# Kernel optimization log

Measured on AMD Instinct MI355X. Metric: run time of the kernel, lower is better.

Reference implementation:

```python
import jax, jax.numpy as jnp
import numpy as np

NUM_HEADS = 4
MIN_NORM = 1e-8


def setup_inputs() -> dict:
    key = jax.random.key(0)
    k1, k2 = jax.random.split(key)
    N, D = 4096, 129  # D = out_channels + 1 (Lorentz time coord + space)
    query_input = jax.random.normal(k1, (N, D), dtype=jnp.float32)
    source_input = jax.random.normal(k2, (N, D), dtype=jnp.float32)
    scale = jnp.full((1,), np.sqrt(128.0), dtype=jnp.float32)  # sqrt(out_channels)
    bias = jnp.zeros((), dtype=jnp.float32)
    return {"query_input": query_input, "source_input": source_input,
            "scale": scale, "bias": bias}


def _lorentz_self_inner(x):
    # <x,x>_L = -x0^2 + ||x_rest||^2, keepdim on last axis
    return -x[..., :1] ** 2 + jnp.sum(x[..., 1:] ** 2, axis=-1, keepdims=True)


def _mid_point_normalize(ave):
    # mid_point denominator: sqrt(clamp_min(|-<ave,ave>_L|, 1e-8))
    denom = jnp.sqrt(jnp.clip(jnp.abs(-_lorentz_self_inner(ave)), MIN_NORM, None))
    return ave / denom


def reference(query_input, source_input, scale, bias):
    H = NUM_HEADS
    N, D = query_input.shape
    # stack identical copies per head (module stacks the raw inputs H times)
    q = jnp.broadcast_to(query_input[None], (H, N, D))   # [H,N,D]
    k = jnp.broadcast_to(source_input[None], (H, N, D))  # [H,N,D]
    v = k
    # cinner: negate time component of q, then matmul with k^T
    qm = jnp.concatenate([-q[..., :1], q[..., 1:]], axis=-1)
    att = 2.0 + 2.0 * jnp.einsum('hnd,hmd->hnm', qm, k)  # [H,N,N]
    att = att / scale + bias
    att = jax.nn.softmax(att, axis=-1)
    # mid_point with weights: ave = att @ v, then Lorentz normalization
    ave = jnp.einsum('hnm,hmd->hnd', att, v)              # [H,N,D]
    out = _mid_point_normalize(ave)
    # transpose to [N,H,D], mid_point without weights = mean over heads
    out = jnp.transpose(out, (1, 0, 2))                   # [N,H,D]
    ave2 = jnp.mean(out, axis=-2)                         # [N,D]
    return _mid_point_normalize(ave2)
```

## Files before the change

kernel.cpp:

```cpp
#include <hip/hip_runtime.h>
#include <math.h>


typedef __attribute__((ext_vector_type(8))) _Float16 f16x8;
typedef __attribute__((ext_vector_type(8))) short short8;
typedef __attribute__((ext_vector_type(4))) float f32x4;

#define NQ 4096
#define DD 129
#define BM 16
#define NWAVE 8
#define NT 512
#define TILE 32
#define NSPLIT 2
#define KVSEG (NQ / NSPLIT)
#define NSTEP (KVSEG / (NWAVE * TILE))
#define NQG (NQ / BM)

#define WS_KH   ((size_t)0)
#define WS_VT   ((size_t)1 << 20)
#define WS_K128 ((size_t)2 << 20)
#define WS_OP   ((size_t)3 << 20)
#define WS_MLA  ((size_t)7 << 20)

__device__ __forceinline__ short f2h_bits(float x) {
  _Float16 h = (_Float16)x;
  return *reinterpret_cast<short*>(&h);
}

__global__ __launch_bounds__(256) void prepass(
    const float* __restrict__ Kg,
    short* __restrict__ Kh, short* __restrict__ VT, float* __restrict__ K128)
{
  __shared__ short tile[32][128];
  const int t  = threadIdx.x;
  const int j0 = blockIdx.x * 32;

#pragma unroll
  for (int i = 0; i < 2; ++i) {
    const int idx = t + 256 * i;
    const int r   = idx >> 4;
    const int d0  = (idx & 15) * 8;
    const float* src = Kg + (size_t)(j0 + r) * DD + d0;
    short8 sv;
#pragma unroll
    for (int e = 0; e < 8; ++e) {
      const short s = f2h_bits(src[e]);
      sv[e] = s;
      tile[r][d0 + e] = s;
    }
    *reinterpret_cast<short8*>(Kh + (size_t)(j0 + r) * 128 + d0) = sv;
  }
  if (t < 32) K128[j0 + t] = Kg[(size_t)(j0 + t) * DD + 128];
  __syncthreads();

  {
    const int d = t >> 1, half = t & 1;
    short v[16];
#pragma unroll
    for (int i = 0; i < 16; ++i) {
      const int p = 16 * half + i;
      const int g = p >> 3, e = p & 7;
      const int j = (e < 4) ? (4 * g + e) : (16 + 4 * g + (e - 4));
      v[i] = tile[j][d];
    }
    short8 s0, s1;
#pragma unroll
    for (int i = 0; i < 8; ++i) { s0[i] = v[i]; s1[i] = v[8 + i]; }
    short* dst = VT + (size_t)d * NQ + j0 + 16 * half;
    *reinterpret_cast<short8*>(dst)     = s0;
    *reinterpret_cast<short8*>(dst + 8) = s1;
  }
}

__global__ __launch_bounds__(NT, 4) void attn_split(
    const float* __restrict__ Qg,
    const short* __restrict__ Kh, const short* __restrict__ VT,
    const float* __restrict__ K128,
    const float* __restrict__ scale_p, const float* __restrict__ bias_p,
    float* __restrict__ OP, float* __restrict__ MLA)
{
  __shared__ float OwS[4][BM * 128];
  __shared__ float mS[NWAVE][BM], lS[NWAVE][BM], aS[NWAVE][BM];

  const int bid = blockIdx.x;
  const int xcd = bid & 7;
  const int sp  = xcd & 1;
  const int qg  = ((xcd >> 1) << 6) + (bid >> 3);

  const int tid  = threadIdx.x;
  const int wid  = tid >> 6;
  const int lane = tid & 63;
  const int g    = lane >> 4;
  const int c    = lane & 15;
  const int row0 = qg * BM;

  const float sA = 2.0f / scale_p[0];
  const float sB = sA + bias_p[0];

  f16x8 qf[4];
  const int qrow = row0 + c;
  const float q128 = Qg[(size_t)qrow * DD + 128];
#pragma unroll
  for (int cc = 0; cc < 4; ++cc) {
#pragma unroll
    for (int e = 0; e < 8; ++e) {
      const int d = 32 * cc + 8 * g + e;
      float v = Qg[(size_t)qrow * DD + d];
      if (d == 0) v = -v;
      qf[cc][e] = (_Float16)v;
    }
  }

  f32x4 accO[8];
#pragma unroll
  for (int i = 0; i < 8; ++i) accO[i] = (f32x4){0.f, 0.f, 0.f, 0.f};
  float m_run = -INFINITY, l_run = 0.f, a128 = 0.f;

  for (int t = 0; t < NSTEP; ++t) {
    const int j0 = sp * KVSEG + (t * NWAVE + wid) * TILE;
    const int rA = j0 + c, rB = rA + 16;

    f16x8 vf[8];
#pragma unroll
    for (int dt = 0; dt < 8; ++dt)
      vf[dt] = *reinterpret_cast<const f16x8*>(
          VT + (size_t)(dt * 16 + c) * NQ + j0 + 8 * g);

    const f32x4 kk1 = *reinterpret_cast<const f32x4*>(K128 + j0 + 4 * g);
    const f32x4 kk2 = *reinterpret_cast<const f32x4*>(K128 + j0 + 16 + 4 * g);

    f32x4 s1acc = (f32x4){0.f, 0.f, 0.f, 0.f};
    f32x4 s2acc = (f32x4){0.f, 0.f, 0.f, 0.f};
    const short* KA = Kh + (size_t)rA * 128 + 8 * g;
    const short* KB = Kh + (size_t)rB * 128 + 8 * g;
#pragma unroll
    for (int cc = 0; cc < 4; ++cc)
      s1acc = __builtin_amdgcn_mfma_f32_16x16x32_f16(
          *reinterpret_cast<const f16x8*>(KA + 32 * cc), qf[cc], s1acc, 0, 0, 0);
#pragma unroll
    for (int cc = 0; cc < 4; ++cc)
      s2acc = __builtin_amdgcn_mfma_f32_16x16x32_f16(
          *reinterpret_cast<const f16x8*>(KB + 32 * cc), qf[cc], s2acc, 0, 0, 0);

    float s1[4], s2[4];
#pragma unroll
    for (int r = 0; r < 4; ++r) {
      s1[r] = (s1acc[r] + q128 * kk1[r]) * sA + sB;
      s2[r] = (s2acc[r] + q128 * kk2[r]) * sA + sB;
    }
    float tmax = fmaxf(fmaxf(fmaxf(s1[0], s1[1]), fmaxf(s1[2], s1[3])),
                       fmaxf(fmaxf(s2[0], s2[1]), fmaxf(s2[2], s2[3])));
    tmax = fmaxf(tmax, __shfl_xor(tmax, 16));
    tmax = fmaxf(tmax, __shfl_xor(tmax, 32));
    const float m_old = m_run;
    const float m_new = fmaxf(m_old, tmax);

    float p1[4], p2[4], tsum = 0.f;
#pragma unroll
    for (int r = 0; r < 4; ++r) {
      p1[r] = __expf(s1[r] - m_new);
      p2[r] = __expf(s2[r] - m_new);
      tsum += p1[r] + p2[r];
    }
    tsum += __shfl_xor(tsum, 16);
    tsum += __shfl_xor(tsum, 32);
    const float alpha = __expf(m_old - m_new);
    l_run = l_run * alpha + tsum;
    m_run = m_new;

    float dp = 0.f;
#pragma unroll
    for (int r = 0; r < 4; ++r) dp += p1[r] * kk1[r] + p2[r] * kk2[r];
    a128 = a128 * alpha + dp;

    if (__any(m_new > m_old)) {
      float ar[4];
#pragma unroll
      for (int r = 0; r < 4; ++r) ar[r] = __shfl(alpha, 4 * g + r);
#pragma unroll
      for (int dt = 0; dt < 8; ++dt)
#pragma unroll
        for (int r = 0; r < 4; ++r) accO[dt][r] *= ar[r];
    }

    f16x8 pa;
#pragma unroll
    for (int r = 0; r < 4; ++r) {
      pa[r]     = (_Float16)p1[r];
      pa[4 + r] = (_Float16)p2[r];
    }

#pragma unroll
    for (int dt = 0; dt < 8; ++dt)
      accO[dt] = __builtin_amdgcn_mfma_f32_16x16x32_f16(pa, vf[dt], accO[dt], 0, 0, 0);
  }

  a128 += __shfl_xor(a128, 16);
  a128 += __shfl_xor(a128, 32);
  if (lane < 16) mS[wid][lane] = m_run;
  __syncthreads();

  float M = mS[0][c];
#pragma unroll
  for (int w = 1; w < NWAVE; ++w) M = fmaxf(M, mS[w][c]);
  const float ew = __expf(m_run - M);
  if (lane < 16) { lS[wid][lane] = l_run * ew; aS[wid][lane] = a128 * ew; }

  float ewr[4];
#pragma unroll
  for (int r = 0; r < 4; ++r) ewr[r] = __shfl(ew, 4 * g + r);
#pragma unroll
  for (int dt = 0; dt < 8; ++dt)
#pragma unroll
    for (int r = 0; r < 4; ++r) accO[dt][r] *= ewr[r];

  if (wid < 4) {
#pragma unroll
    for (int dt = 0; dt < 8; ++dt)
#pragma unroll
      for (int r = 0; r < 4; ++r)
        OwS[wid][(4 * g + r) * 128 + dt * 16 + c] = accO[dt][r];
  }
  __syncthreads();
  if (wid >= 4) {
#pragma unroll
    for (int dt = 0; dt < 8; ++dt)
#pragma unroll
      for (int r = 0; r < 4; ++r)
        OwS[wid - 4][(4 * g + r) * 128 + dt * 16 + c] += accO[dt][r];
  }
  __syncthreads();

  {
    const int q = tid >> 5, s = tid & 31;
    f32x4 o = *reinterpret_cast<const f32x4*>(&OwS[0][q * 128 + 4 * s]);
#pragma unroll
    for (int i = 1; i < 4; ++i) {
      const f32x4 oi = *reinterpret_cast<const f32x4*>(&OwS[i][q * 128 + 4 * s]);
#pragma unroll
      for (int e = 0; e < 4; ++e) o[e] += oi[e];
    }
    float L = 0.f, A = 0.f, Mq = -INFINITY;
#pragma unroll
    for (int w = 0; w < NWAVE; ++w) {
      L += lS[w][q]; A += aS[w][q]; Mq = fmaxf(Mq, mS[w][q]);
    }
    float* dst = OP + ((size_t)(qg * NSPLIT + sp) * BM + q) * 128 + 4 * s;
    *reinterpret_cast<f32x4*>(dst) = o;
    if (s == 0) {
      float* mla = MLA + (size_t)(qg * NSPLIT + sp) * 48;
      mla[q] = Mq; mla[16 + q] = L; mla[32 + q] = A;
    }
  }
}

__global__ __launch_bounds__(256) void merge_norm(
    const float* __restrict__ OP, const float* __restrict__ MLA,
    float* __restrict__ outg)
{
  const int qg  = blockIdx.x;
  const int rq  = threadIdx.x >> 4;
  const int seg = threadIdx.x & 15;

  const float* a0 = MLA + (size_t)(qg * NSPLIT + 0) * 48;
  const float* a1 = MLA + (size_t)(qg * NSPLIT + 1) * 48;
  const float m1 = a0[rq], l1 = a0[16 + rq], A1 = a0[32 + rq];
  const float m2 = a1[rq], l2 = a1[16 + rq], A2 = a1[32 + rq];
  const float M  = fmaxf(m1, m2);
  const float w1 = __expf(m1 - M), w2 = __expf(m2 - M);
  const float invL = 1.0f / (w1 * l1 + w2 * l2);

  const float* O1 = OP + ((size_t)(qg * NSPLIT + 0) * BM + rq) * 128 + 8 * seg;
  const float* O2 = OP + ((size_t)(qg * NSPLIT + 1) * BM + rq) * 128 + 8 * seg;
  float o[8];
#pragma unroll
  for (int i = 0; i < 8; ++i) o[i] = (w1 * O1[i] + w2 * O2[i]) * invL;
  const float A = (w1 * A1 + w2 * A2) * invL;

  float part = 0.f;
#pragma unroll
  for (int i = 0; i < 8; ++i) part += o[i] * o[i];
  if (seg == 0) part += -2.f * o[0] * o[0] + A * A;
  part += __shfl_xor(part, 1);
  part += __shfl_xor(part, 2);
  part += __shfl_xor(part, 4);
  part += __shfl_xor(part, 8);
  const float den1 = sqrtf(fmaxf(fabsf(part), 1e-8f));

  float y[8];
#pragma unroll
  for (int i = 0; i < 8; ++i) y[i] = o[i] / den1;
  const float yA = A / den1;

  float p2 = 0.f;
#pragma unroll
  for (int i = 0; i < 8; ++i) p2 += y[i] * y[i];
  if (seg == 0) p2 += -2.f * y[0] * y[0] + yA * yA;
  p2 += __shfl_xor(p2, 1);
  p2 += __shfl_xor(p2, 2);
  p2 += __shfl_xor(p2, 4);
  p2 += __shfl_xor(p2, 8);
  const float den2 = sqrtf(fmaxf(fabsf(p2), 1e-8f));

  float* orow = outg + (size_t)(qg * BM + rq) * DD;
#pragma unroll
  for (int i = 0; i < 8; ++i) orow[8 * seg + i] = y[i] / den2;
  if (seg == 0) orow[128] = yA / den2;
}

extern "C" void kernel_launch(void* const* d_in, const int* in_sizes, int n_in,
                              void* d_out, int out_size, void* d_ws, size_t ws_size,
                              hipStream_t stream) {
  const float* Qg = (const float*)d_in[0];
  const float* Kg = (const float*)d_in[1];
  const float* sc = (const float*)d_in[2];
  const float* bs = (const float*)d_in[3];
  float* out = (float*)d_out;

  char* ws = (char*)d_ws;
  short* Kh   = (short*)(ws + WS_KH);
  short* VT   = (short*)(ws + WS_VT);
  float* K128 = (float*)(ws + WS_K128);
  float* OP   = (float*)(ws + WS_OP);
  float* MLA  = (float*)(ws + WS_MLA);

  hipLaunchKernelGGL(prepass, dim3(NQ / 32), dim3(256), 0, stream, Kg, Kh, VT, K128);
  hipLaunchKernelGGL(attn_split, dim3(NQG * NSPLIT), dim3(NT), 0, stream,
                     Qg, Kh, VT, K128, sc, bs, OP, MLA);
  hipLaunchKernelGGL(merge_norm, dim3(NQG), dim3(256), 0, stream, OP, MLA, out);
}
```

Before: 133.7 us.

## Fuse split-KV merge into attention via atomic counter and add 4-way split

Removes the separate merge_norm kernel: each attention block bumps a per-query-group atomic counter, and the last block to finish merges the partial softmax statistics and applies both Lorentz normalizations. The prepass now also converts Q to fp16, with the time coordinate negated, and splits work across more blocks. The KV split becomes a template and switches to 4 splits when workspace allows, with launch bounds raised to 8 waves per EU. This trades a kernel launch and a pass over the partials for a memset, threadfence and atomic overhead, plus possible register pressure from the higher occupancy target.

```diff
diff --git a/kernel.cpp b/kernel.cpp
--- a/kernel.cpp
+++ b/kernel.cpp
@@ -12,16 +12,17 @@
 #define NWAVE 8
 #define NT 512
 #define TILE 32
-#define NSPLIT 2
-#define KVSEG (NQ / NSPLIT)
-#define NSTEP (KVSEG / (NWAVE * TILE))
 #define NQG (NQ / BM)
 
 #define WS_KH   ((size_t)0)
 #define WS_VT   ((size_t)1 << 20)
-#define WS_K128 ((size_t)2 << 20)
-#define WS_OP   ((size_t)3 << 20)
-#define WS_MLA  ((size_t)7 << 20)
+#define WS_QH   ((size_t)2 << 20)
+#define WS_K128 ((size_t)3 << 20)
+#define WS_Q128 (((size_t)3 << 20) + (16 << 10))
+#define WS_MLA  (((size_t)3 << 20) + (32 << 10))
+#define WS_CNT  (((size_t)3 << 20) + (224 << 10))
+#define WS_OP   (((size_t)3 << 20) + (256 << 10))
+#define NEED(nsplit) (WS_OP + (size_t)(nsplit) * (NQG * BM * 128 * 4))
 
 __device__ __forceinline__ short f2h_bits(float x) {
   _Float16 h = (_Float16)x;
@@ -29,64 +30,74 @@
 }
 
 __global__ __launch_bounds__(256) void prepass(
-    const float* __restrict__ Kg,
-    short* __restrict__ Kh, short* __restrict__ VT, float* __restrict__ K128)
+    const float* __restrict__ Kg, const float* __restrict__ Qg,
+    short* __restrict__ Kh, short* __restrict__ Qh, short* __restrict__ VT,
+    float* __restrict__ K128, float* __restrict__ Q128)
 {
-  __shared__ short tile[32][128];
+  __shared__ short tile[32][72];
+  const int bx  = blockIdx.x;
+  const int isQ = blockIdx.y;
+  const int jg = bx >> 1, dh = bx & 1;
+  const int j0 = jg * 32, d0 = dh * 64;
+  const float* src = isQ ? Qg : Kg;
+  short* plane = isQ ? Qh : Kh;
+
   const int t  = threadIdx.x;
-  const int j0 = blockIdx.x * 32;
-
-#pragma unroll
-  for (int i = 0; i < 2; ++i) {
-    const int idx = t + 256 * i;
-    const int r   = idx >> 4;
-    const int d0  = (idx & 15) * 8;
-    const float* src = Kg + (size_t)(j0 + r) * DD + d0;
+  const int r  = t >> 3;
+  const int e0 = (t & 7) * 8;
+
+  {
+    const float* s = src + (size_t)(j0 + r) * DD + d0 + e0;
     short8 sv;
 #pragma unroll
     for (int e = 0; e < 8; ++e) {
-      const short s = f2h_bits(src[e]);
-      sv[e] = s;
-      tile[r][d0 + e] = s;
-    }
-    *reinterpret_cast<short8*>(Kh + (size_t)(j0 + r) * 128 + d0) = sv;
-  }
-  if (t < 32) K128[j0 + t] = Kg[(size_t)(j0 + t) * DD + 128];
+      float v = s[e];
+      if (isQ && dh == 0 && e0 == 0 && e == 0) v = -v;
+      sv[e] = f2h_bits(v);
+    }
+    *reinterpret_cast<short8*>(&tile[r][e0]) = sv;
+    *reinterpret_cast<short8*>(plane + (size_t)(j0 + r) * 128 + d0 + e0) = sv;
+  }
+  if (dh == 0 && t < 32) {
+    const float v = src[(size_t)(j0 + t) * DD + 128];
+    (isQ ? Q128 : K128)[j0 + t] = v;
+  }
+  if (isQ) return;
   __syncthreads();
 
   {
-    const int d = t >> 1, half = t & 1;
-    short v[16];
-#pragma unroll
-    for (int i = 0; i < 16; ++i) {
-      const int p = 16 * half + i;
-      const int g = p >> 3, e = p & 7;
-      const int j = (e < 4) ? (4 * g + e) : (16 + 4 * g + (e - 4));
-      v[i] = tile[j][d];
-    }
-    short8 s0, s1;
-#pragma unroll
-    for (int i = 0; i < 8; ++i) { s0[i] = v[i]; s1[i] = v[8 + i]; }
-    short* dst = VT + (size_t)d * NQ + j0 + 16 * half;
-    *reinterpret_cast<short8*>(dst)     = s0;
-    *reinterpret_cast<short8*>(dst + 8) = s1;
+    const int dl = t >> 2, q8 = t & 3;
+    short8 sv;
+#pragma unroll
+    for (int e = 0; e < 8; ++e) {
+      const int j = (e < 4) ? (4 * q8 + e) : (16 + 4 * q8 + (e - 4));
+      sv[e] = tile[j][dl];
+    }
+    *reinterpret_cast<short8*>(VT + (size_t)(d0 + dl) * NQ + j0 + q8 * 8) = sv;
   }
 }
 
-__global__ __launch_bounds__(NT, 4) void attn_split(
-    const float* __restrict__ Qg,
+template <int NSPLIT>
+__global__ __launch_bounds__(NT, 8) void attn_fused(
+    const short* __restrict__ Qh, const float* __restrict__ Q128,
     const short* __restrict__ Kh, const short* __restrict__ VT,
     const float* __restrict__ K128,
     const float* __restrict__ scale_p, const float* __restrict__ bias_p,
-    float* __restrict__ OP, float* __restrict__ MLA)
+    float* __restrict__ OP, float* __restrict__ MLA, int* __restrict__ cnt,
+    float* __restrict__ outg)
 {
+  constexpr int KVSEG = NQ / NSPLIT;
+  constexpr int NSTEP = KVSEG / (NWAVE * TILE);
+  constexpr int XPS   = 8 / NSPLIT;
+
   __shared__ float OwS[4][BM * 128];
   __shared__ float mS[NWAVE][BM], lS[NWAVE][BM], aS[NWAVE][BM];
+  __shared__ int lastS;
 
   const int bid = blockIdx.x;
   const int xcd = bid & 7;
-  const int sp  = xcd & 1;
-  const int qg  = ((xcd >> 1) << 6) + (bid >> 3);
+  const int sp  = xcd / XPS;
+  const int qg  = (xcd % XPS) * (NQG / XPS) + (bid >> 3);
 
   const int tid  = threadIdx.x;
   const int wid  = tid >> 6;
@@ -98,19 +109,12 @@
   const float sA = 2.0f / scale_p[0];
   const float sB = sA + bias_p[0];
 
+  const int qrow = row0 + c;
   f16x8 qf[4];
-  const int qrow = row0 + c;
-  const float q128 = Qg[(size_t)qrow * DD + 128];
-#pragma unroll
-  for (int cc = 0; cc < 4; ++cc) {
-#pragma unroll
-    for (int e = 0; e < 8; ++e) {
-      const int d = 32 * cc + 8 * g + e;
-      float v = Qg[(size_t)qrow * DD + d];
-      if (d == 0) v = -v;
-      qf[cc][e] = (_Float16)v;
-    }
-  }
+#pragma unroll
+  for (int cc = 0; cc < 4; ++cc)
+    qf[cc] = *reinterpret_cast<const f16x8*>(Qh + (size_t)qrow * 128 + 32 * cc + 8 * g);
+  const float q128 = Q128[qrow];
 
   f32x4 accO[8];
 #pragma unroll
@@ -253,60 +257,71 @@
       mla[q] = Mq; mla[16 + q] = L; mla[32 + q] = A;
     }
   }
-}
-
-__global__ __launch_bounds__(256) void merge_norm(
-    const float* __restrict__ OP, const float* __restrict__ MLA,
-    float* __restrict__ outg)
-{
-  const int qg  = blockIdx.x;
-  const int rq  = threadIdx.x >> 4;
-  const int seg = threadIdx.x & 15;
-
-  const float* a0 = MLA + (size_t)(qg * NSPLIT + 0) * 48;
-  const float* a1 = MLA + (size_t)(qg * NSPLIT + 1) * 48;
-  const float m1 = a0[rq], l1 = a0[16 + rq], A1 = a0[32 + rq];
-  const float m2 = a1[rq], l2 = a1[16 + rq], A2 = a1[32 + rq];
-  const float M  = fmaxf(m1, m2);
-  const float w1 = __expf(m1 - M), w2 = __expf(m2 - M);
-  const float invL = 1.0f / (w1 * l1 + w2 * l2);
-
-  const float* O1 = OP + ((size_t)(qg * NSPLIT + 0) * BM + rq) * 128 + 8 * seg;
-  const float* O2 = OP + ((size_t)(qg * NSPLIT + 1) * BM + rq) * 128 + 8 * seg;
-  float o[8];
-#pragma unroll
-  for (int i = 0; i < 8; ++i) o[i] = (w1 * O1[i] + w2 * O2[i]) * invL;
-  const float A = (w1 * A1 + w2 * A2) * invL;
-
-  float part = 0.f;
-#pragma unroll
-  for (int i = 0; i < 8; ++i) part += o[i] * o[i];
-  if (seg == 0) part += -2.f * o[0] * o[0] + A * A;
-  part += __shfl_xor(part, 1);
-  part += __shfl_xor(part, 2);
-  part += __shfl_xor(part, 4);
-  part += __shfl_xor(part, 8);
-  const float den1 = sqrtf(fmaxf(fabsf(part), 1e-8f));
-
-  float y[8];
-#pragma unroll
-  for (int i = 0; i < 8; ++i) y[i] = o[i] / den1;
-  const float yA = A / den1;
-
-  float p2 = 0.f;
-#pragma unroll
-  for (int i = 0; i < 8; ++i) p2 += y[i] * y[i];
-  if (seg == 0) p2 += -2.f * y[0] * y[0] + yA * yA;
-  p2 += __shfl_xor(p2, 1);
-  p2 += __shfl_xor(p2, 2);
-  p2 += __shfl_xor(p2, 4);
-  p2 += __shfl_xor(p2, 8);
-  const float den2 = sqrtf(fmaxf(fabsf(p2), 1e-8f));
-
-  float* orow = outg + (size_t)(qg * BM + rq) * DD;
-#pragma unroll
-  for (int i = 0; i < 8; ++i) orow[8 * seg + i] = y[i] / den2;
-  if (seg == 0) orow[128] = yA / den2;
+
+  __syncthreads();
+  if (tid == 0) {
+    __threadfence();
+    const int old = atomicAdd(&cnt[qg], 1);
+    lastS = (old == NSPLIT - 1);
+  }
+  __syncthreads();
+  if (!lastS) return;
+  __threadfence();
+
+  {
+    const int rq = tid >> 5, seg = tid & 31;
+    float mm[NSPLIT];
+    float Mq = -INFINITY;
+#pragma unroll
+    for (int w = 0; w < NSPLIT; ++w) {
+      mm[w] = MLA[(size_t)(qg * NSPLIT + w) * 48 + rq];
+      Mq = fmaxf(Mq, mm[w]);
+    }
+    float L = 0.f, A = 0.f;
+    float o[4] = {0.f, 0.f, 0.f, 0.f};
+#pragma unroll
+    for (int w = 0; w < NSPLIT; ++w) {
+      const float* mla = MLA + (size_t)(qg * NSPLIT + w) * 48;
+      const float eww = __expf(mm[w] - Mq);
+      L += eww * mla[16 + rq];
+      A += eww * mla[32 + rq];
+      const float* Opw = OP + ((size_t)(qg * NSPLIT + w) * BM + rq) * 128 + 4 * seg;
+#pragma unroll
+      for (int i = 0; i < 4; ++i) o[i] += eww * Opw[i];
+    }
+    const float invL = 1.0f / L;
+#pragma unroll
+    for (int i = 0; i < 4; ++i) o[i] *= invL;
+    A *= invL;
+
+    float part = o[0] * o[0] + o[1] * o[1] + o[2] * o[2] + o[3] * o[3];
+    if (seg == 0) part += -2.f * o[0] * o[0] + A * A;
+    part += __shfl_xor(part, 1);
+    part += __shfl_xor(part, 2);
+    part += __shfl_xor(part, 4);
+    part += __shfl_xor(part, 8);
+    part += __shfl_xor(part, 16);
+    const float den1 = sqrtf(fmaxf(fabsf(part), 1e-8f));
+
+    float y[4];
+#pragma unroll
+    for (int i = 0; i < 4; ++i) y[i] = o[i] / den1;
+    const float yA = A / den1;
+
+    float p2 = y[0] * y[0] + y[1] * y[1] + y[2] * y[2] + y[3] * y[3];
+    if (seg == 0) p2 += -2.f * y[0] * y[0] + yA * yA;
+    p2 += __shfl_xor(p2, 1);
+    p2 += __shfl_xor(p2, 2);
+    p2 += __shfl_xor(p2, 4);
+    p2 += __shfl_xor(p2, 8);
+    p2 += __shfl_xor(p2, 16);
+    const float den2 = sqrtf(fmaxf(fabsf(p2), 1e-8f));
+
+    float* orow = outg + (size_t)(row0 + rq) * DD;
+#pragma unroll
+    for (int i = 0; i < 4; ++i) orow[4 * seg + i] = y[i] / den2;
+    if (seg == 0) orow[128] = yA / den2;
+  }
 }
 
 extern "C" void kernel_launch(void* const* d_in, const int* in_sizes, int n_in,
@@ -321,12 +336,21 @@
   char* ws = (char*)d_ws;
   short* Kh   = (short*)(ws + WS_KH);
   short* VT   = (short*)(ws + WS_VT);
+  short* Qh   = (short*)(ws + WS_QH);
   float* K128 = (float*)(ws + WS_K128);
+  float* Q128 = (float*)(ws + WS_Q128);
+  float* MLA  = (float*)(ws + WS_MLA);
+  int*   cnt  = (int*)(ws + WS_CNT);
   float* OP   = (float*)(ws + WS_OP);
-  float* MLA  = (float*)(ws + WS_MLA);
-
-  hipLaunchKernelGGL(prepass, dim3(NQ / 32), dim3(256), 0, stream, Kg, Kh, VT, K128);
-  hipLaunchKernelGGL(attn_split, dim3(NQG * NSPLIT), dim3(NT), 0, stream,
-                     Qg, Kh, VT, K128, sc, bs, OP, MLA);
-  hipLaunchKernelGGL(merge_norm, dim3(NQG), dim3(256), 0, stream, OP, MLA, out);
+
+  hipMemsetAsync(cnt, 0, NQG * sizeof(int), stream);
+  hipLaunchKernelGGL(prepass, dim3(256, 2), dim3(256), 0, stream,
+                     Kg, Qg, Kh, Qh, VT, K128, Q128);
+  if (ws_size >= NEED(4) + (1 << 20)) {
+    hipLaunchKernelGGL((attn_fused<4>), dim3(NQG * 4), dim3(NT), 0, stream,
+                       Qh, Q128, Kh, VT, K128, sc, bs, OP, MLA, cnt, out);
+  } else {
+    hipLaunchKernelGGL((attn_fused<2>), dim3(NQG * 2), dim3(NT), 0, stream,
+                       Qh, Q128, Kh, VT, K128, sc, bs, OP, MLA, cnt, out);
+  }
 }
```

Result: slower. 496.5 us (+271.2%).

## Precompute fp16 Q in prepass, hoist K loads ahead of MFMAs, relax launch bounds

Applied to the files above, without the earlier changes.

The prepass now also converts Q to an fp16 plane with the time coordinate pre-negated, plus a separate Q128 column. The attention kernel then loads Q with vector loads instead of per-element strided fp32 loads and conversions. The prepass grid is split across two d-halves and a Q/K axis, which shrinks the shared tile. In the main loop all K fragments are loaded before the MFMAs, with a sched_barrier to keep the loads issued early. Launch bounds drop from 4 to 2 blocks per SM minimum, allowing more registers at the possible cost of occupancy.

```diff
diff --git a/kernel.cpp b/kernel.cpp
--- a/kernel.cpp
+++ b/kernel.cpp
@@ -19,62 +19,69 @@
 
 #define WS_KH   ((size_t)0)
 #define WS_VT   ((size_t)1 << 20)
-#define WS_K128 ((size_t)2 << 20)
-#define WS_OP   ((size_t)3 << 20)
-#define WS_MLA  ((size_t)7 << 20)
+#define WS_QH   ((size_t)2 << 20)
+#define WS_K128 ((size_t)3 << 20)
+#define WS_Q128 (((size_t)3 << 20) + (16 << 10))
+#define WS_MLA  (((size_t)3 << 20) + (32 << 10))
+#define WS_OP   ((size_t)4 << 20)
 
 __device__ __forceinline__ short f2h_bits(float x) {
   _Float16 h = (_Float16)x;
   return *reinterpret_cast<short*>(&h);
 }
 
+#define MF(a, b, cacc) __builtin_amdgcn_mfma_f32_16x16x32_f16(a, b, cacc, 0, 0, 0)
+
 __global__ __launch_bounds__(256) void prepass(
-    const float* __restrict__ Kg,
-    short* __restrict__ Kh, short* __restrict__ VT, float* __restrict__ K128)
+    const float* __restrict__ Kg, const float* __restrict__ Qg,
+    short* __restrict__ Kh, short* __restrict__ Qh, short* __restrict__ VT,
+    float* __restrict__ K128, float* __restrict__ Q128)
 {
-  __shared__ short tile[32][128];
+  __shared__ short tile[32][72];
+  const int bx  = blockIdx.x;
+  const int isQ = blockIdx.y;
+  const int jg = bx >> 1, dh = bx & 1;
+  const int j0 = jg * 32, d0 = dh * 64;
+  const float* src = isQ ? Qg : Kg;
+  short* plane = isQ ? Qh : Kh;
+
   const int t  = threadIdx.x;
-  const int j0 = blockIdx.x * 32;
-
-#pragma unroll
-  for (int i = 0; i < 2; ++i) {
-    const int idx = t + 256 * i;
-    const int r   = idx >> 4;
-    const int d0  = (idx & 15) * 8;
-    const float* src = Kg + (size_t)(j0 + r) * DD + d0;
+  const int r  = t >> 3;
+  const int e0 = (t & 7) * 8;
+
+  {
+    const float* s = src + (size_t)(j0 + r) * DD + d0 + e0;
     short8 sv;
 #pragma unroll
     for (int e = 0; e < 8; ++e) {
-      const short s = f2h_bits(src[e]);
-      sv[e] = s;
-      tile[r][d0 + e] = s;
-    }
-    *reinterpret_cast<short8*>(Kh + (size_t)(j0 + r) * 128 + d0) = sv;
-  }
-  if (t < 32) K128[j0 + t] = Kg[(size_t)(j0 + t) * DD + 128];
+      float v = s[e];
+      if (isQ && dh == 0 && e0 == 0 && e == 0) v = -v;
+      sv[e] = f2h_bits(v);
+    }
+    *reinterpret_cast<short8*>(&tile[r][e0]) = sv;
+    *reinterpret_cast<short8*>(plane + (size_t)(j0 + r) * 128 + d0 + e0) = sv;
+  }
+  if (dh == 0 && t < 32) {
+    const float v = src[(size_t)(j0 + t) * DD + 128];
+    (isQ ? Q128 : K128)[j0 + t] = v;
+  }
+  if (isQ) return;
   __syncthreads();
 
   {
-    const int d = t >> 1, half = t & 1;
-    short v[16];
-#pragma unroll
-    for (int i = 0; i < 16; ++i) {
-      const int p = 16 * half + i;
-      const int g = p >> 3, e = p & 7;
-      const int j = (e < 4) ? (4 * g + e) : (16 + 4 * g + (e - 4));
-      v[i] = tile[j][d];
-    }
-    short8 s0, s1;
-#pragma unroll
-    for (int i = 0; i < 8; ++i) { s0[i] = v[i]; s1[i] = v[8 + i]; }
-    short* dst = VT + (size_t)d * NQ + j0 + 16 * half;
-    *reinterpret_cast<short8*>(dst)     = s0;
-    *reinterpret_cast<short8*>(dst + 8) = s1;
-  }
-}
-
-__global__ __launch_bounds__(NT, 4) void attn_split(
-    const float* __restrict__ Qg,
+    const int dl = t >> 2, q8 = t & 3;
+    short8 sv;
+#pragma unroll
+    for (int e = 0; e < 8; ++e) {
+      const int j = (e < 4) ? (4 * q8 + e) : (16 + 4 * q8 + (e - 4));
+      sv[e] = tile[j][dl];
+    }
+    *reinterpret_cast<short8*>(VT + (size_t)(d0 + dl) * NQ + j0 + q8 * 8) = sv;
+  }
+}
+
+__global__ __launch_bounds__(NT, 2) void attn_split(
+    const short* __restrict__ Qh, const float* __restrict__ Q128,
     const short* __restrict__ Kh, const short* __restrict__ VT,
     const float* __restrict__ K128,
     const float* __restrict__ scale_p, const float* __restrict__ bias_p,
@@ -87,6 +94,7 @@
   const int xcd = bid & 7;
   const int sp  = xcd & 1;
   const int qg  = ((xcd >> 1) << 6) + (bid >> 3);
+  const int spBase = sp * KVSEG;
 
   const int tid  = threadIdx.x;
   const int wid  = tid >> 6;
@@ -98,19 +106,12 @@
   const float sA = 2.0f / scale_p[0];
   const float sB = sA + bias_p[0];
 
+  const int qrow = row0 + c;
   f16x8 qf[4];
-  const int qrow = row0 + c;
-  const float q128 = Qg[(size_t)qrow * DD + 128];
-#pragma unroll
-  for (int cc = 0; cc < 4; ++cc) {
-#pragma unroll
-    for (int e = 0; e < 8; ++e) {
-      const int d = 32 * cc + 8 * g + e;
-      float v = Qg[(size_t)qrow * DD + d];
-      if (d == 0) v = -v;
-      qf[cc][e] = (_Float16)v;
-    }
-  }
+#pragma unroll
+  for (int cc = 0; cc < 4; ++cc)
+    qf[cc] = *reinterpret_cast<const f16x8*>(Qh + (size_t)qrow * 128 + 32 * cc + 8 * g);
+  const float q128 = Q128[qrow];
 
   f32x4 accO[8];
 #pragma unroll
@@ -118,30 +119,30 @@
   float m_run = -INFINITY, l_run = 0.f, a128 = 0.f;
 
   for (int t = 0; t < NSTEP; ++t) {
-    const int j0 = sp * KVSEG + (t * NWAVE + wid) * TILE;
-    const int rA = j0 + c, rB = rA + 16;
-
-    f16x8 vf[8];
+    const int j0 = spBase + (t * NWAVE + wid) * TILE;
+
+    f16x8 vf[8], ka[4], kb[4];
 #pragma unroll
     for (int dt = 0; dt < 8; ++dt)
       vf[dt] = *reinterpret_cast<const f16x8*>(
           VT + (size_t)(dt * 16 + c) * NQ + j0 + 8 * g);
-
+    const short* KA = Kh + (size_t)(j0 + c) * 128 + 8 * g;
+    const short* KB = Kh + (size_t)(j0 + 16 + c) * 128 + 8 * g;
+#pragma unroll
+    for (int cc = 0; cc < 4; ++cc) {
+      ka[cc] = *reinterpret_cast<const f16x8*>(KA + 32 * cc);
+      kb[cc] = *reinterpret_cast<const f16x8*>(KB + 32 * cc);
+    }
     const f32x4 kk1 = *reinterpret_cast<const f32x4*>(K128 + j0 + 4 * g);
     const f32x4 kk2 = *reinterpret_cast<const f32x4*>(K128 + j0 + 16 + 4 * g);
+    __builtin_amdgcn_sched_barrier(0);
 
     f32x4 s1acc = (f32x4){0.f, 0.f, 0.f, 0.f};
     f32x4 s2acc = (f32x4){0.f, 0.f, 0.f, 0.f};
-    const short* KA = Kh + (size_t)rA * 128 + 8 * g;
-    const short* KB = Kh + (size_t)rB * 128 + 8 * g;
-#pragma unroll
-    for (int cc = 0; cc < 4; ++cc)
-      s1acc = __builtin_amdgcn_mfma_f32_16x16x32_f16(
-          *reinterpret_cast<const f16x8*>(KA + 32 * cc), qf[cc], s1acc, 0, 0, 0);
-#pragma unroll
-    for (int cc = 0; cc < 4; ++cc)
-      s2acc = __builtin_amdgcn_mfma_f32_16x16x32_f16(
-          *reinterpret_cast<const f16x8*>(KB + 32 * cc), qf[cc], s2acc, 0, 0, 0);
+#pragma unroll
+    for (int cc = 0; cc < 4; ++cc) s1acc = MF(ka[cc], qf[cc], s1acc);
+#pragma unroll
+    for (int cc = 0; cc < 4; ++cc) s2acc = MF(kb[cc], qf[cc], s2acc);
 
     float s1[4], s2[4];
 #pragma unroll
@@ -193,7 +194,7 @@
 
 #pragma unroll
     for (int dt = 0; dt < 8; ++dt)
-      accO[dt] = __builtin_amdgcn_mfma_f32_16x16x32_f16(pa, vf[dt], accO[dt], 0, 0, 0);
+      accO[dt] = MF(pa, vf[dt], accO[dt]);
   }
 
   a128 += __shfl_xor(a128, 16);
@@ -321,12 +322,15 @@
   char* ws = (char*)d_ws;
   short* Kh   = (short*)(ws + WS_KH);
   short* VT   = (short*)(ws + WS_VT);
+  short* Qh   = (short*)(ws + WS_QH);
   float* K128 = (float*)(ws + WS_K128);
+  float* Q128 = (float*)(ws + WS_Q128);
+  float* MLA  = (float*)(ws + WS_MLA);
   float* OP   = (float*)(ws + WS_OP);
-  float* MLA  = (float*)(ws + WS_MLA);
-
-  hipLaunchKernelGGL(prepass, dim3(NQ / 32), dim3(256), 0, stream, Kg, Kh, VT, K128);
+
+  hipLaunchKernelGGL(prepass, dim3(256, 2), dim3(256), 0, stream,
+                     Kg, Qg, Kh, Qh, VT, K128, Q128);
   hipLaunchKernelGGL(attn_split, dim3(NQG * NSPLIT), dim3(NT), 0, stream,
-                     Qg, Kh, VT, K128, sc, bs, OP, MLA);
+                     Qh, Q128, Kh, VT, K128, sc, bs, OP, MLA);
   hipLaunchKernelGGL(merge_norm, dim3(NQG), dim3(256), 0, stream, OP, MLA, out);
 }
```

Result: slower. 138.3 us (+3.4%).
